# Performance work log

Measured on AMD Instinct MI355X. Metric: run time of the kernel, lower is better.

## Reference

```python
import jax, jax.numpy as jnp
import numpy as np

N = 8192        # batch of samples
CODE_LEN = 128  # codeword length
NUM_CLASSES = 1000
THRESHOLD = 0.5
EPS = 1e-4


def setup_inputs() -> dict:
    key = jax.random.key(0)
    k1, k2, k3 = jax.random.split(key, 3)
    # probabilities strictly inside (0,1) so BCE logs are finite
    output = jax.random.uniform(k1, (N, CODE_LEN), dtype=jnp.float32,
                                minval=EPS, maxval=1.0 - EPS)
    # binary ECOC codeword table
    codewords = jax.random.randint(k2, (NUM_CLASSES, CODE_LEN), 0, 2).astype(jnp.float32)
    target = jax.random.randint(k3, (N,), 0, NUM_CLASSES, dtype=jnp.int64)
    return {"output": output, "codewords": codewords, "target": target}


def reference(output, codewords, target):
    # gather the target codewords: [N, C]
    cw_t = codewords[target]
    # elementwise BCE with reduction='none'
    bce = -(cw_t * jnp.log(output) + (1.0 - cw_t) * jnp.log1p(-output))
    # no-grad branch: hard predictions and pairwise Hamming distances
    pred = (output > THRESHOLD).astype(output.dtype)  # binary {0,1}
    # cdist p=0 counts mismatched coordinates; for binary vectors x,y:
    #   hamming(x,y) = sum(x) + sum(y) - 2 * x.y   (exact, GEMM-mappable)
    sp = jnp.sum(pred, axis=-1)   # [N]
    sc = jnp.sum(cw_t, axis=-1)   # [N]
    ham = sp[:, None] + sc[None, :] - 2.0 * (pred @ cw_t.T)  # [N, N]
    sigma = jax.lax.stop_gradient(jnp.min(ham, axis=1))      # [N]
    weighted = bce + sigma[:, None]
    return jnp.mean(weighted)
```

## Files before the change

### kernel.cpp

```cpp
#include <hip/hip_runtime.h>

#define N_SAMPLES   8192
#define CODE_LEN    128
#define NUM_CLASSES 1000

__global__ __launch_bounds__(256) void pack_kernel(
        const float* __restrict__ codewords, uint4* __restrict__ cw_packed) {
    const int w = threadIdx.x >> 6, l = threadIdx.x & 63;
    const int c = blockIdx.x * 4 + w;
    if (c < NUM_CLASSES) {
        float v0 = codewords[c * CODE_LEN + l];
        float v1 = codewords[c * CODE_LEN + 64 + l];
        unsigned long long b0 = __ballot(v0 > 0.5f);
        unsigned long long b1 = __ballot(v1 > 0.5f);
        if (l == 0)
            cw_packed[c] = make_uint4((unsigned)b0, (unsigned)(b0 >> 32),
                                      (unsigned)b1, (unsigned)(b1 >> 32));
    }
}

__global__ __launch_bounds__(256) void main_kernel(
        const float* __restrict__ output, const float* __restrict__ codewords,
        const int* __restrict__ target, const uint4* __restrict__ cw_packed,
        float* __restrict__ out) {
    __shared__ float    wbce[4];
    __shared__ unsigned wsig[4];
    const int tid = threadIdx.x;
    const int w   = tid >> 6;
    const int l   = tid & 63;
    const int b   = blockIdx.x;

    float bce = 0.f;
    uint4 pred[2];
    #pragma unroll
    for (int j = 0; j < 2; ++j) {
        const int i = b * 8 + w * 2 + j;
        const int t = target[i];
        float o0 = output[i * CODE_LEN + l];
        float o1 = output[i * CODE_LEN + 64 + l];
        float c0 = codewords[t * CODE_LEN + l];
        float c1 = codewords[t * CODE_LEN + 64 + l];
        bce += (c0 > 0.5f ? -__logf(o0) : -__logf(1.0f - o0))
             + (c1 > 0.5f ? -__logf(o1) : -__logf(1.0f - o1));
        unsigned long long p0 = __ballot(o0 > 0.5f);
        unsigned long long p1 = __ballot(o1 > 0.5f);
        pred[j] = make_uint4((unsigned)p0, (unsigned)(p0 >> 32),
                             (unsigned)p1, (unsigned)(p1 >> 32));
    }
    #pragma unroll
    for (int m = 1; m <= 32; m <<= 1) bce += __shfl_xor(bce, m);
    if (l == 0) wbce[w] = bce;

    unsigned best0 = 0xFFFFFFFFu, best1 = 0xFFFFFFFFu;
    for (int c = l; c < NUM_CLASSES; c += 64) {
        uint4 cw = cw_packed[c];
        unsigned d0 = __popc(pred[0].x ^ cw.x) + __popc(pred[0].y ^ cw.y)
                    + __popc(pred[0].z ^ cw.z) + __popc(pred[0].w ^ cw.w);
        unsigned d1 = __popc(pred[1].x ^ cw.x) + __popc(pred[1].y ^ cw.y)
                    + __popc(pred[1].z ^ cw.z) + __popc(pred[1].w ^ cw.w);
        best0 = min(best0, d0);
        best1 = min(best1, d1);
    }
    #pragma unroll
    for (int m = 1; m <= 32; m <<= 1) {
        best0 = min(best0, (unsigned)__shfl_xor((int)best0, m));
        best1 = min(best1, (unsigned)__shfl_xor((int)best1, m));
    }
    if (l == 0) wsig[w] = best0 + best1;
    __syncthreads();

    if (tid == 0) {
        float    fb = wbce[0] + wbce[1] + wbce[2] + wbce[3];
        unsigned fs = wsig[0] + wsig[1] + wsig[2] + wsig[3];
        atomicAdd(out, fb / (float)(N_SAMPLES * CODE_LEN)
                     + (float)fs / (float)N_SAMPLES);
    }
}

extern "C" void kernel_launch(void* const* d_in, const int* in_sizes, int n_in,
                              void* d_out, int out_size, void* d_ws, size_t ws_size,
                              hipStream_t stream) {
    const float* output    = (const float*)d_in[0];
    const float* codewords = (const float*)d_in[1];
    const int*   target    = (const int*)d_in[2];
    float*       out       = (float*)d_out;
    uint4*       cw_packed = (uint4*)d_ws;

    pack_kernel<<<250, 256, 0, stream>>>(codewords, cw_packed);
    main_kernel<<<N_SAMPLES / 8, 256, 0, stream>>>(
        output, codewords, target, cw_packed, out);
}
```

Baseline: 77.12 us.

## Replace per-block atomicAdd with partial buffers and a deterministic finalize kernel

Each main-kernel block now writes its BCE and sigma partial sums to workspace arrays, and a new single-block 1024-thread kernel reduces them and writes the output. This removes 1024 contended float atomics on a single address. The diff also computes one log per element by selecting the log argument before calling it. The cost is an extra kernel launch and a serial dependency on the finalize step. The output is now written directly rather than accumulated, so it no longer relies on being pre-zeroed.

```diff
diff --git a/kernel.cpp b/kernel.cpp
--- a/kernel.cpp
+++ b/kernel.cpp
@@ -3,6 +3,7 @@
 #define N_SAMPLES   8192
 #define CODE_LEN    128
 #define NUM_CLASSES 1000
+#define MAINBLK     1024
 
 __global__ __launch_bounds__(256) void pack_kernel(
         const float* __restrict__ codewords, uint4* __restrict__ cw_packed) {
@@ -22,7 +23,7 @@
 __global__ __launch_bounds__(256) void main_kernel(
         const float* __restrict__ output, const float* __restrict__ codewords,
         const int* __restrict__ target, const uint4* __restrict__ cw_packed,
-        float* __restrict__ out) {
+        float* __restrict__ bce_part, unsigned* __restrict__ sig_part) {
     __shared__ float    wbce[4];
     __shared__ unsigned wsig[4];
     const int tid = threadIdx.x;
@@ -40,8 +41,9 @@
         float o1 = output[i * CODE_LEN + 64 + l];
         float c0 = codewords[t * CODE_LEN + l];
         float c1 = codewords[t * CODE_LEN + 64 + l];
-        bce += (c0 > 0.5f ? -__logf(o0) : -__logf(1.0f - o0))
-             + (c1 > 0.5f ? -__logf(o1) : -__logf(1.0f - o1));
+        float a0 = (c0 > 0.5f) ? o0 : 1.0f - o0;
+        float a1 = (c1 > 0.5f) ? o1 : 1.0f - o1;
+        bce -= __logf(a0) + __logf(a1);
         unsigned long long p0 = __ballot(o0 > 0.5f);
         unsigned long long p1 = __ballot(o1 > 0.5f);
         pred[j] = make_uint4((unsigned)p0, (unsigned)(p0 >> 32),
@@ -70,10 +72,33 @@
     __syncthreads();
 
     if (tid == 0) {
-        float    fb = wbce[0] + wbce[1] + wbce[2] + wbce[3];
-        unsigned fs = wsig[0] + wsig[1] + wsig[2] + wsig[3];
-        atomicAdd(out, fb / (float)(N_SAMPLES * CODE_LEN)
-                     + (float)fs / (float)N_SAMPLES);
+        bce_part[b] = wbce[0] + wbce[1] + wbce[2] + wbce[3];
+        sig_part[b] = wsig[0] + wsig[1] + wsig[2] + wsig[3];
+    }
+}
+
+__global__ __launch_bounds__(1024) void finalize_kernel(
+        const float* __restrict__ bce_part, const unsigned* __restrict__ sig_part,
+        float* __restrict__ out) {
+    __shared__ float    fb16[16];
+    __shared__ unsigned fs16[16];
+    const int tid = threadIdx.x;
+    const int w   = tid >> 6, l = tid & 63;
+    float    fb = bce_part[tid];
+    unsigned fs = sig_part[tid];
+    #pragma unroll
+    for (int m = 1; m <= 32; m <<= 1) {
+        fb += __shfl_xor(fb, m);
+        fs += (unsigned)__shfl_xor((int)fs, m);
+    }
+    if (l == 0) { fb16[w] = fb; fs16[w] = fs; }
+    __syncthreads();
+    if (tid == 0) {
+        float    tb = 0.f;
+        unsigned ts = 0u;
+        #pragma unroll
+        for (int k = 0; k < 16; ++k) { tb += fb16[k]; ts += fs16[k]; }
+        out[0] = tb / (float)(N_SAMPLES * CODE_LEN) + (float)ts / (float)N_SAMPLES;
     }
 }
 
@@ -84,9 +109,13 @@
     const float* codewords = (const float*)d_in[1];
     const int*   target    = (const int*)d_in[2];
     float*       out       = (float*)d_out;
-    uint4*       cw_packed = (uint4*)d_ws;
+
+    float*    bce_part  = (float*)d_ws;
+    unsigned* sig_part  = (unsigned*)((char*)d_ws + 4096);
+    uint4*    cw_packed = (uint4*)((char*)d_ws + 16384);
 
     pack_kernel<<<250, 256, 0, stream>>>(codewords, cw_packed);
-    main_kernel<<<N_SAMPLES / 8, 256, 0, stream>>>(
-        output, codewords, target, cw_packed, out);
+    main_kernel<<<MAINBLK, 256, 0, stream>>>(
+        output, codewords, target, cw_packed, bce_part, sig_part);
+    finalize_kernel<<<1, 1024, 0, stream>>>(bce_part, sig_part, out);
 }
```

Result: faster. 66.37 us (-13.9%).
